# Kernel tuning notes

Hardware: AMD Instinct MI355X
Metric: run time of the kernel (lower is better)

Reference implementation:

```python
import jax, jax.numpy as jnp
import numpy as np

BS, NE, F = 128, 512, 6
HEADS, DPH = 4, 4
N_EMBD = HEADS * DPH  # 16


def setup_inputs() -> dict:
    key = jax.random.key(0)
    k_inp, k_mask, kq, kk, kv, kp = jax.random.split(key, 6)
    inp = jax.random.normal(k_inp, (BS, NE, F), dtype=jnp.float32)
    # binary float mask; guarantee at least one unmasked entity per batch row
    mask = (jax.random.uniform(k_mask, (BS, NE)) < 0.8).astype(jnp.float32)
    mask = mask.at[:, 0].set(1.0)
    std = 1.0 / np.sqrt(N_EMBD)
    Wq = jax.random.normal(kq, (N_EMBD, F), dtype=jnp.float32) * std
    Wk = jax.random.normal(kk, (N_EMBD, F), dtype=jnp.float32) * std
    Wv = jax.random.normal(kv, (N_EMBD, F), dtype=jnp.float32) * std
    Wpost = jax.random.normal(kp, (F, N_EMBD), dtype=jnp.float32) * std
    return {"inp": inp, "mask": mask, "Wq": Wq, "Wk": Wk, "Wv": Wv, "Wpost": Wpost}


def reference(inp, mask, Wq, Wk, Wv, Wpost):
    bs, ne, f = inp.shape
    x_in = inp * mask[:, :, None]                       # mask input entities
    # projections (Linear with weight [out,in]): x @ W.T
    q = (x_in @ Wq.T).reshape(bs, ne, HEADS, DPH)
    k = (x_in @ Wk.T).reshape(bs, ne, HEADS, DPH)
    v = (x_in @ Wv.T).reshape(bs, ne, HEADS, DPH)
    scale = 1.0 / np.sqrt(N_EMBD / HEADS)               # 1/sqrt(4)
    logits = jnp.einsum('bqhd,bkhd->bhqk', q, k) * scale  # [bs,H,NE,NE]
    logits = logits + 1e9 * (mask[:, None, None, :] - 1.0)  # mask keys pre-softmax
    p = jax.nn.softmax(logits, axis=-1)
    p = p * mask[:, None, :, None]                      # zero masked query rows
    att = jnp.einsum('bhqk,bkhd->bqhd', p, v).reshape(bs, ne, N_EMBD)
    x = x_in + att @ Wpost.T                            # residual
    # mask-corrected mean/std normalization over dims [1,2]
    N = jnp.sum(mask, axis=1)[:, None, None]            # [bs,1,1] valid entity count
    mu = jnp.mean(x, axis=(1, 2), keepdims=True) * (ne / N)
    x2 = x + (1.0 - mask[:, :, None]) * mu              # fill masked slots with mu
    m2 = jnp.mean(x2, axis=(1, 2), keepdims=True)
    var = jnp.sum((x2 - m2) ** 2, axis=(1, 2), keepdims=True) / (ne * f - 1)  # unbiased
    std = jnp.sqrt(var) * jnp.sqrt((f * ne - 1.0) / (f * N - 1.0))
    xn = (x - mu) / (std + 1e-6)
    # masked mean pool over entities
    summed = jnp.sum(xn * mask[:, :, None], axis=1)     # [bs,F]
    denom = jnp.sum(mask, axis=1)[:, None]
    return summed / denom
```

## Files before the change

### kernel.cpp

```cpp
#include <hip/hip_runtime.h>
#include <math.h>

#define BS    128
#define NE    512
#define F     6
#define NH    4
#define DPH   4
#define NEMBD 16

#define CH    8
#define CPAD  65

#if __has_builtin(__builtin_amdgcn_exp2f)
#define EXP2(x) __builtin_amdgcn_exp2f(x)
#else
#define EXP2(x) exp2f(x)
#endif

typedef float v2f __attribute__((ext_vector_type(2)));

__global__ __launch_bounds__(512) void attn_kernel(
    const float* __restrict__ inp, const float* __restrict__ mask,
    const float* __restrict__ Wq, const float* __restrict__ Wk,
    const float* __restrict__ Wv, float* __restrict__ att_out)
{
    const int b    = blockIdx.x >> 2;
    const int h    = blockIdx.x & 3;
    const int t    = threadIdx.x;
    const int c    = t & 7;
    const int g    = t >> 3;
    const int w    = t >> 6;
    const int lane = t & 63;

    __shared__ float4 sk[CH * CPAD];
    __shared__ float4 sv[CH * CPAD];
    __shared__ float4 sq[576];
    __shared__ unsigned short rlist[512];
    __shared__ int wcnt[8];

    const float4 z4 = make_float4(0.f, 0.f, 0.f, 0.f);
    sk[c * CPAD + g] = z4;
    sv[c * CPAD + g] = z4;
    sq[9 * g + c]    = z4;

    const float me = mask[b * NE + t];
    const bool act = me > 0.f;

    const unsigned long long ball = __ballot(act);
    const int prefix = __builtin_amdgcn_mbcnt_hi((unsigned int)(ball >> 32),
                        __builtin_amdgcn_mbcnt_lo((unsigned int)ball, 0));
    if (lane == 0) wcnt[w] = (int)__popcll(ball);

    __syncthreads();

    int base = 0, Nk = 0;
    #pragma unroll
    for (int u = 0; u < 8; ++u) {
        const int cu = wcnt[u];
        Nk += cu;
        if (u < w) base += cu;
    }
    const int L = (Nk + 7) >> 3;
    const float lcorr = (float)(8 * L - Nk);

    if (act) {
        const int s = base + prefix;
        const float2* rp = (const float2*)(inp + ((size_t)(b * NE + t)) * F);
        const float2 r0 = rp[0], r1 = rp[1], r2 = rp[2];
        const float x0 = r0.x, x1 = r0.y, x2 = r1.x,
                    x3 = r1.y, x4 = r2.x, x5 = r2.y;
        const float* wk = Wk + h * DPH * F;
        const float* wv = Wv + h * DPH * F;
        const float* wq = Wq + h * DPH * F;
        const float QS = 0.5f * 1.44269504088896340736f;
        float kk[4], vv[4], qq[4];
        #pragma unroll
        for (int d = 0; d < DPH; ++d) {
            const float* wd = wk + d * F;
            kk[d] = x0*wd[0] + x1*wd[1] + x2*wd[2] + x3*wd[3] + x4*wd[4] + x5*wd[5];
            wd = wv + d * F;
            vv[d] = x0*wd[0] + x1*wd[1] + x2*wd[2] + x3*wd[3] + x4*wd[4] + x5*wd[5];
            wd = wq + d * F;
            qq[d] = QS * (x0*wd[0] + x1*wd[1] + x2*wd[2] + x3*wd[3] + x4*wd[4] + x5*wd[5]);
        }
        sk[(s & 7) * CPAD + (s >> 3)] = make_float4(kk[0], kk[1], kk[2], kk[3]);
        sv[(s & 7) * CPAD + (s >> 3)] = make_float4(vv[0], vv[1], vv[2], vv[3]);
        sq[9 * (s >> 3) + (s & 7)]    = make_float4(qq[0], qq[1], qq[2], qq[3]);
        rlist[s] = (unsigned short)t;
    }

    __syncthreads();

    if (64 * w >= Nk) return;

    float4 qa[8];
    #pragma unroll
    for (int r = 0; r < 8; ++r) qa[r] = sq[9 * g + r];
    v2f qv[4][DPH];
    #pragma unroll
    for (int p = 0; p < 4; ++p) {
        qv[p][0] = (v2f){qa[2*p].x, qa[2*p+1].x};
        qv[p][1] = (v2f){qa[2*p].y, qa[2*p+1].y};
        qv[p][2] = (v2f){qa[2*p].z, qa[2*p+1].z};
        qv[p][3] = (v2f){qa[2*p].w, qa[2*p+1].w};
    }

    const float4* kb = sk + c * CPAD;
    const float4* vb = sv + c * CPAD;
    v2f l2[4], a2[4][DPH];
    #pragma unroll
    for (int p = 0; p < 4; ++p) {
        l2[p] = (v2f)(0.f);
        #pragma unroll
        for (int d = 0; d < DPH; ++d) a2[p][d] = (v2f)(0.f);
    }

    #pragma unroll 4
    for (int j = 0; j < L; ++j) {
        const float4 kv = kb[j];
        const float4 uv = vb[j];
        const v2f kx = (v2f){kv.x, kv.x}, ky = (v2f){kv.y, kv.y},
                  kz = (v2f){kv.z, kv.z}, kw = (v2f){kv.w, kv.w};
        const v2f ux = (v2f){uv.x, uv.x}, uy = (v2f){uv.y, uv.y},
                  uz = (v2f){uv.z, uv.z}, uw = (v2f){uv.w, uv.w};
        #pragma unroll
        for (int p = 0; p < 4; ++p) {
            v2f s = qv[p][3] * kw;
            s = __builtin_elementwise_fma(qv[p][2], kz, s);
            s = __builtin_elementwise_fma(qv[p][1], ky, s);
            s = __builtin_elementwise_fma(qv[p][0], kx, s);
            v2f e;
            e.x = EXP2(s.x);
            e.y = EXP2(s.y);
            l2[p] += e;
            a2[p][0] = __builtin_elementwise_fma(e, ux, a2[p][0]);
            a2[p][1] = __builtin_elementwise_fma(e, uy, a2[p][1]);
            a2[p][2] = __builtin_elementwise_fma(e, uz, a2[p][2]);
            a2[p][3] = __builtin_elementwise_fma(e, uw, a2[p][3]);
        }
    }

    const int b0 = c & 1, b1 = (c >> 1) & 1, b2 = (c >> 2) & 1;

    float k1[5][4];
    #pragma unroll
    for (int p = 0; p < 4; ++p) {
        {
            const v2f v = l2[p];
            const float snd = b0 ? v.x : v.y;
            k1[0][p] = (b0 ? v.y : v.x) + __shfl_xor(snd, 1);
        }
        #pragma unroll
        for (int d = 0; d < DPH; ++d) {
            const v2f v = a2[p][d];
            const float snd = b0 ? v.x : v.y;
            k1[1 + d][p] = (b0 ? v.y : v.x) + __shfl_xor(snd, 1);
        }
    }

    float k2[5][2];
    #pragma unroll
    for (int v = 0; v < 5; ++v) {
        #pragma unroll
        for (int q = 0; q < 2; ++q) {
            const float keep = b1 ? k1[v][2*q + 1] : k1[v][2*q];
            const float snd  = b1 ? k1[v][2*q]     : k1[v][2*q + 1];
            k2[v][q] = keep + __shfl_xor(snd, 2);
        }
    }

    float fin[5];
    #pragma unroll
    for (int v = 0; v < 5; ++v) {
        const float keep = b2 ? k2[v][1] : k2[v][0];
        const float snd  = b2 ? k2[v][0] : k2[v][1];
        fin[v] = keep + __shfl_xor(snd, 4);
    }

    const int slot = 8 * g + c;
    if (slot < Nk) {
        const int row = rlist[slot];
        const float rs = 1.0f / (fin[0] - lcorr);
        float4* o = (float4*)(att_out + ((size_t)(b * NE + row)) * NEMBD + h * DPH);
        *o = make_float4(fin[1] * rs, fin[2] * rs, fin[3] * rs, fin[4] * rs);
    }
}

__global__ __launch_bounds__(NE) void epi_kernel(
    const float* __restrict__ inp, const float* __restrict__ mask,
    const float* __restrict__ Wpost, const float* __restrict__ att,
    float* __restrict__ out)
{
    const int b = blockIdx.x;
    const int i = threadIdx.x;
    const int wave = i >> 6;
    const int lane = i & 63;

    __shared__ float swp[F * NEMBD];
    __shared__ float red[64];

    if (i < F * NEMBD) swp[i] = Wpost[i];
    __syncthreads();

    const float mi = mask[b * NE + i];
    const float* row = inp + ((size_t)(b * NE + i)) * F;
    const float* ar  = att + ((size_t)(b * NE + i)) * NEMBD;

    float a[NEMBD];
    #pragma unroll
    for (int t = 0; t < NEMBD; t += 4) {
        const float4 v = *(const float4*)(ar + t);
        a[t] = v.x * mi; a[t+1] = v.y * mi; a[t+2] = v.z * mi; a[t+3] = v.w * mi;
    }

    float x[F];
    #pragma unroll
    for (int f = 0; f < F; ++f) {
        float acc = row[f] * mi;
        #pragma unroll
        for (int t = 0; t < NEMBD; ++t) acc = fmaf(a[t], swp[f * NEMBD + t], acc);
        x[f] = acc;
    }

    float rsum = x[0] + x[1] + x[2] + x[3] + x[4] + x[5];
    float rn = mi;
    #pragma unroll
    for (int off = 32; off >= 1; off >>= 1) {
        rsum += __shfl_down(rsum, off);
        rn   += __shfl_down(rn, off);
    }
    if (lane == 0) { red[wave * 2] = rsum; red[wave * 2 + 1] = rn; }
    __syncthreads();
    float S = 0.f, N = 0.f;
    #pragma unroll
    for (int w = 0; w < 8; ++w) { S += red[w * 2]; N += red[w * 2 + 1]; }

    const float mu     = S / (6.0f * N);
    const float sum_x2 = S + (NE - N) * 6.0f * mu;
    const float m2     = sum_x2 / (NE * 6.0f);
    const float add    = (1.0f - mi) * mu;

    float ss = 0.f;
    #pragma unroll
    for (int f = 0; f < F; ++f) { const float d = x[f] + add - m2; ss = fmaf(d, d, ss); }

    __syncthreads();
    #pragma unroll
    for (int off = 32; off >= 1; off >>= 1) ss += __shfl_down(ss, off);
    if (lane == 0) red[wave] = ss;
    __syncthreads();
    float vs = 0.f;
    #pragma unroll
    for (int w = 0; w < 8; ++w) vs += red[w];

    const float var  = vs / (NE * 6.0f - 1.0f);
    const float stdv = sqrtf(var) * sqrtf((6.0f * NE - 1.0f) / (6.0f * N - 1.0f));
    const float inv  = 1.0f / (stdv + 1e-6f);

    float y[F];
    #pragma unroll
    for (int f = 0; f < F; ++f) y[f] = mi * (x[f] - mu) * inv;

    __syncthreads();
    #pragma unroll
    for (int off = 32; off >= 1; off >>= 1) {
        #pragma unroll
        for (int f = 0; f < F; ++f) y[f] += __shfl_down(y[f], off);
    }
    if (lane == 0) {
        #pragma unroll
        for (int f = 0; f < F; ++f) red[wave * F + f] = y[f];
    }
    __syncthreads();
    if (i < F) {
        float tt = 0.f;
        #pragma unroll
        for (int w = 0; w < 8; ++w) tt += red[w * F + i];
        out[b * F + i] = tt / N;
    }
}

extern "C" void kernel_launch(void* const* d_in, const int* in_sizes, int n_in,
                              void* d_out, int out_size, void* d_ws, size_t ws_size,
                              hipStream_t stream) {
    const float* inp   = (const float*)d_in[0];
    const float* mask  = (const float*)d_in[1];
    const float* Wq    = (const float*)d_in[2];
    const float* Wk    = (const float*)d_in[3];
    const float* Wv    = (const float*)d_in[4];
    const float* Wpost = (const float*)d_in[5];
    float* out = (float*)d_out;
    float* att = (float*)d_ws;

    attn_kernel<<<BS * NH, 512, 0, stream>>>(inp, mask, Wq, Wk, Wv, att);
    epi_kernel <<<BS, NE, 0, stream>>>(inp, mask, Wpost, att, out);
}
```

Baseline: 94.74 us.

## Fuse epilogue into attention kernel via last-block atomic counter per batch

Merges the attention and epilogue kernels into one launch. Each of the four head blocks per batch writes its attention output, then bumps an atomic counter, and the last block to finish runs the post-projection, normalization and pooling. The attention workspace is relaid out head-major so each head writes a contiguous slab. This removes a kernel launch and the inter-kernel gap, but adds a memset launch, thread fences, and a serialized epilogue tail on the last-arriving block.

```diff
diff --git a/kernel.cpp b/kernel.cpp
--- a/kernel.cpp
+++ b/kernel.cpp
@@ -19,10 +19,12 @@
 
 typedef float v2f __attribute__((ext_vector_type(2)));
 
-__global__ __launch_bounds__(512) void attn_kernel(
+__global__ __launch_bounds__(512) void attn_fused(
     const float* __restrict__ inp, const float* __restrict__ mask,
     const float* __restrict__ Wq, const float* __restrict__ Wk,
-    const float* __restrict__ Wv, float* __restrict__ att_out)
+    const float* __restrict__ Wv, const float* __restrict__ Wpost,
+    float* __restrict__ att, int* __restrict__ done,
+    float* __restrict__ out)
 {
     const int b    = blockIdx.x >> 2;
     const int h    = blockIdx.x & 3;
@@ -37,6 +39,9 @@
     __shared__ float4 sq[576];
     __shared__ unsigned short rlist[512];
     __shared__ int wcnt[8];
+    __shared__ int slast;
+    __shared__ float swp[F * NEMBD];
+    __shared__ float red[64];
 
     const float4 z4 = make_float4(0.f, 0.f, 0.f, 0.f);
     sk[c * CPAD + g] = z4;
@@ -91,126 +96,125 @@
 
     __syncthreads();
 
-    if (64 * w >= Nk) return;
-
-    float4 qa[8];
-    #pragma unroll
-    for (int r = 0; r < 8; ++r) qa[r] = sq[9 * g + r];
-    v2f qv[4][DPH];
-    #pragma unroll
-    for (int p = 0; p < 4; ++p) {
-        qv[p][0] = (v2f){qa[2*p].x, qa[2*p+1].x};
-        qv[p][1] = (v2f){qa[2*p].y, qa[2*p+1].y};
-        qv[p][2] = (v2f){qa[2*p].z, qa[2*p+1].z};
-        qv[p][3] = (v2f){qa[2*p].w, qa[2*p+1].w};
-    }
-
-    const float4* kb = sk + c * CPAD;
-    const float4* vb = sv + c * CPAD;
-    v2f l2[4], a2[4][DPH];
-    #pragma unroll
-    for (int p = 0; p < 4; ++p) {
-        l2[p] = (v2f)(0.f);
-        #pragma unroll
-        for (int d = 0; d < DPH; ++d) a2[p][d] = (v2f)(0.f);
-    }
-
-    #pragma unroll 4
-    for (int j = 0; j < L; ++j) {
-        const float4 kv = kb[j];
-        const float4 uv = vb[j];
-        const v2f kx = (v2f){kv.x, kv.x}, ky = (v2f){kv.y, kv.y},
-                  kz = (v2f){kv.z, kv.z}, kw = (v2f){kv.w, kv.w};
-        const v2f ux = (v2f){uv.x, uv.x}, uy = (v2f){uv.y, uv.y},
-                  uz = (v2f){uv.z, uv.z}, uw = (v2f){uv.w, uv.w};
+    if (64 * w < Nk) {
+        float4 qa[8];
+        #pragma unroll
+        for (int r = 0; r < 8; ++r) qa[r] = sq[9 * g + r];
+        v2f qv[4][DPH];
         #pragma unroll
         for (int p = 0; p < 4; ++p) {
-            v2f s = qv[p][3] * kw;
-            s = __builtin_elementwise_fma(qv[p][2], kz, s);
-            s = __builtin_elementwise_fma(qv[p][1], ky, s);
-            s = __builtin_elementwise_fma(qv[p][0], kx, s);
-            v2f e;
-            e.x = EXP2(s.x);
-            e.y = EXP2(s.y);
-            l2[p] += e;
-            a2[p][0] = __builtin_elementwise_fma(e, ux, a2[p][0]);
-            a2[p][1] = __builtin_elementwise_fma(e, uy, a2[p][1]);
-            a2[p][2] = __builtin_elementwise_fma(e, uz, a2[p][2]);
-            a2[p][3] = __builtin_elementwise_fma(e, uw, a2[p][3]);
-        }
-    }
-
-    const int b0 = c & 1, b1 = (c >> 1) & 1, b2 = (c >> 2) & 1;
-
-    float k1[5][4];
-    #pragma unroll
-    for (int p = 0; p < 4; ++p) {
-        {
-            const v2f v = l2[p];
-            const float snd = b0 ? v.x : v.y;
-            k1[0][p] = (b0 ? v.y : v.x) + __shfl_xor(snd, 1);
-        }
-        #pragma unroll
-        for (int d = 0; d < DPH; ++d) {
-            const v2f v = a2[p][d];
-            const float snd = b0 ? v.x : v.y;
-            k1[1 + d][p] = (b0 ? v.y : v.x) + __shfl_xor(snd, 1);
-        }
-    }
-
-    float k2[5][2];
-    #pragma unroll
-    for (int v = 0; v < 5; ++v) {
-        #pragma unroll
-        for (int q = 0; q < 2; ++q) {
-            const float keep = b1 ? k1[v][2*q + 1] : k1[v][2*q];
-            const float snd  = b1 ? k1[v][2*q]     : k1[v][2*q + 1];
-            k2[v][q] = keep + __shfl_xor(snd, 2);
-        }
-    }
-
-    float fin[5];
-    #pragma unroll
-    for (int v = 0; v < 5; ++v) {
-        const float keep = b2 ? k2[v][1] : k2[v][0];
-        const float snd  = b2 ? k2[v][0] : k2[v][1];
-        fin[v] = keep + __shfl_xor(snd, 4);
-    }
-
-    const int slot = 8 * g + c;
-    if (slot < Nk) {
-        const int row = rlist[slot];
-        const float rs = 1.0f / (fin[0] - lcorr);
-        float4* o = (float4*)(att_out + ((size_t)(b * NE + row)) * NEMBD + h * DPH);
-        *o = make_float4(fin[1] * rs, fin[2] * rs, fin[3] * rs, fin[4] * rs);
-    }
-}
-
-__global__ __launch_bounds__(NE) void epi_kernel(
-    const float* __restrict__ inp, const float* __restrict__ mask,
-    const float* __restrict__ Wpost, const float* __restrict__ att,
-    float* __restrict__ out)
-{
-    const int b = blockIdx.x;
-    const int i = threadIdx.x;
-    const int wave = i >> 6;
-    const int lane = i & 63;
-
-    __shared__ float swp[F * NEMBD];
-    __shared__ float red[64];
+            qv[p][0] = (v2f){qa[2*p].x, qa[2*p+1].x};
+            qv[p][1] = (v2f){qa[2*p].y, qa[2*p+1].y};
+            qv[p][2] = (v2f){qa[2*p].z, qa[2*p+1].z};
+            qv[p][3] = (v2f){qa[2*p].w, qa[2*p+1].w};
+        }
+
+        const float4* kb = sk + c * CPAD;
+        const float4* vb = sv + c * CPAD;
+        v2f l2[4], a2[4][DPH];
+        #pragma unroll
+        for (int p = 0; p < 4; ++p) {
+            l2[p] = (v2f)(0.f);
+            #pragma unroll
+            for (int d = 0; d < DPH; ++d) a2[p][d] = (v2f)(0.f);
+        }
+
+        #pragma unroll 4
+        for (int j = 0; j < L; ++j) {
+            const float4 kv = kb[j];
+            const float4 uv = vb[j];
+            const v2f kx = (v2f){kv.x, kv.x}, ky = (v2f){kv.y, kv.y},
+                      kz = (v2f){kv.z, kv.z}, kw = (v2f){kv.w, kv.w};
+            const v2f ux = (v2f){uv.x, uv.x}, uy = (v2f){uv.y, uv.y},
+                      uz = (v2f){uv.z, uv.z}, uw = (v2f){uv.w, uv.w};
+            #pragma unroll
+            for (int p = 0; p < 4; ++p) {
+                v2f s = qv[p][3] * kw;
+                s = __builtin_elementwise_fma(qv[p][2], kz, s);
+                s = __builtin_elementwise_fma(qv[p][1], ky, s);
+                s = __builtin_elementwise_fma(qv[p][0], kx, s);
+                v2f e;
+                e.x = EXP2(s.x);
+                e.y = EXP2(s.y);
+                l2[p] += e;
+                a2[p][0] = __builtin_elementwise_fma(e, ux, a2[p][0]);
+                a2[p][1] = __builtin_elementwise_fma(e, uy, a2[p][1]);
+                a2[p][2] = __builtin_elementwise_fma(e, uz, a2[p][2]);
+                a2[p][3] = __builtin_elementwise_fma(e, uw, a2[p][3]);
+            }
+        }
+
+        const int b0 = c & 1, b1 = (c >> 1) & 1, b2 = (c >> 2) & 1;
+
+        float k1[5][4];
+        #pragma unroll
+        for (int p = 0; p < 4; ++p) {
+            {
+                const v2f v = l2[p];
+                const float snd = b0 ? v.x : v.y;
+                k1[0][p] = (b0 ? v.y : v.x) + __shfl_xor(snd, 1);
+            }
+            #pragma unroll
+            for (int d = 0; d < DPH; ++d) {
+                const v2f v = a2[p][d];
+                const float snd = b0 ? v.x : v.y;
+                k1[1 + d][p] = (b0 ? v.y : v.x) + __shfl_xor(snd, 1);
+            }
+        }
+
+        float k2[5][2];
+        #pragma unroll
+        for (int v = 0; v < 5; ++v) {
+            #pragma unroll
+            for (int q = 0; q < 2; ++q) {
+                const float keep = b1 ? k1[v][2*q + 1] : k1[v][2*q];
+                const float snd  = b1 ? k1[v][2*q]     : k1[v][2*q + 1];
+                k2[v][q] = keep + __shfl_xor(snd, 2);
+            }
+        }
+
+        float fin[5];
+        #pragma unroll
+        for (int v = 0; v < 5; ++v) {
+            const float keep = b2 ? k2[v][1] : k2[v][0];
+            const float snd  = b2 ? k2[v][0] : k2[v][1];
+            fin[v] = keep + __shfl_xor(snd, 4);
+        }
+
+        const int slot = 8 * g + c;
+        if (slot < Nk) {
+            const int row = rlist[slot];
+            const float rs = 1.0f / (fin[0] - lcorr);
+            float4* o = (float4*)(att + (((size_t)h * BS + b) * NE + row) * 4);
+            *o = make_float4(fin[1] * rs, fin[2] * rs, fin[3] * rs, fin[4] * rs);
+        }
+    }
+
+    __threadfence();
+    __syncthreads();
+    if (t == 0) {
+        const int old = atomicAdd(&done[b], 1);
+        slast = (old == NH - 1) ? 1 : 0;
+        __threadfence();
+    }
+    __syncthreads();
+    if (!slast) return;
+
+    const int i = t;
+    const int wave = w;
 
     if (i < F * NEMBD) swp[i] = Wpost[i];
     __syncthreads();
 
-    const float mi = mask[b * NE + i];
+    const float mi = me;
     const float* row = inp + ((size_t)(b * NE + i)) * F;
-    const float* ar  = att + ((size_t)(b * NE + i)) * NEMBD;
 
     float a[NEMBD];
     #pragma unroll
-    for (int t = 0; t < NEMBD; t += 4) {
-        const float4 v = *(const float4*)(ar + t);
-        a[t] = v.x * mi; a[t+1] = v.y * mi; a[t+2] = v.z * mi; a[t+3] = v.w * mi;
+    for (int hh = 0; hh < NH; ++hh) {
+        const float4 v = *(const float4*)(att + (((size_t)hh * BS + b) * NE + i) * 4);
+        a[4*hh+0] = v.x * mi; a[4*hh+1] = v.y * mi;
+        a[4*hh+2] = v.z * mi; a[4*hh+3] = v.w * mi;
     }
 
     float x[F];
@@ -218,7 +222,7 @@
     for (int f = 0; f < F; ++f) {
         float acc = row[f] * mi;
         #pragma unroll
-        for (int t = 0; t < NEMBD; ++t) acc = fmaf(a[t], swp[f * NEMBD + t], acc);
+        for (int k = 0; k < NEMBD; ++k) acc = fmaf(a[k], swp[f * NEMBD + k], acc);
         x[f] = acc;
     }
 
@@ -233,7 +237,7 @@
     __syncthreads();
     float S = 0.f, N = 0.f;
     #pragma unroll
-    for (int w = 0; w < 8; ++w) { S += red[w * 2]; N += red[w * 2 + 1]; }
+    for (int u = 0; u < 8; ++u) { S += red[u * 2]; N += red[u * 2 + 1]; }
 
     const float mu     = S / (6.0f * N);
     const float sum_x2 = S + (NE - N) * 6.0f * mu;
@@ -251,7 +255,7 @@
     __syncthreads();
     float vs = 0.f;
     #pragma unroll
-    for (int w = 0; w < 8; ++w) vs += red[w];
+    for (int u = 0; u < 8; ++u) vs += red[u];
 
     const float var  = vs / (NE * 6.0f - 1.0f);
     const float stdv = sqrtf(var) * sqrtf((6.0f * NE - 1.0f) / (6.0f * N - 1.0f));
@@ -275,7 +279,7 @@
     if (i < F) {
         float tt = 0.f;
         #pragma unroll
-        for (int w = 0; w < 8; ++w) tt += red[w * F + i];
+        for (int u = 0; u < 8; ++u) tt += red[u * F + i];
         out[b * F + i] = tt / N;
     }
 }
@@ -290,8 +294,11 @@
     const float* Wv    = (const float*)d_in[4];
     const float* Wpost = (const float*)d_in[5];
     float* out = (float*)d_out;
+
     float* att = (float*)d_ws;
-
-    attn_kernel<<<BS * NH, 512, 0, stream>>>(inp, mask, Wq, Wk, Wv, att);
-    epi_kernel <<<BS, NE, 0, stream>>>(inp, mask, Wpost, att, out);
+    int*   done = (int*)((char*)d_ws + (size_t)NH * BS * NE * 4 * sizeof(float));
+
+    hipMemsetAsync(done, 0, BS * sizeof(int), stream);
+    attn_fused<<<BS * NH, 512, 0, stream>>>(inp, mask, Wq, Wk, Wv, Wpost,
+                                            att, done, out);
 }
```

Measured after the change: 185.0 us. 1.95x slower.
